# Performance work log

Measured on AMD Instinct MI355X. Metric: run time of the kernel, lower is better.

The kernel has to match this reference:

```python
import jax, jax.numpy as jnp
import numpy as np

# FPMA (Mitchell-style) approximate bf16 multiply: a*b is approximated by
# integer-adding the exponent+mantissa bit fields of the two bf16 operands
# and subtracting the exponent bias offset (0x3F80 for bf16). Sign is XOR of
# sign bits. Underflow is flushed to zero; overflow clamped to max finite.
SIGN_MASK = 0x8000
MAG_MASK = 0x7FFF
BIAS_OFF = 0x3F80  # 127 << 7 (bf16 exponent bias in bit position)
MAX_FINITE = 0x7F7F
CHUNK = 4  # rows of the input processed per scan step (bounds the [C,N,K] intermediate)


def _fpma_matmul(x, w):
    """x: [M,K] bf16, w: [N,K] bf16 -> [M,N] fp32 accumulated approximate products."""
    xb = jax.lax.bitcast_convert_type(x, jnp.uint16).astype(jnp.int32)  # [M,K]
    wb = jax.lax.bitcast_convert_type(w, jnp.uint16).astype(jnp.int32)  # [N,K]
    M, K = xb.shape
    xs, xm = xb & SIGN_MASK, xb & MAG_MASK
    ws, wm = wb & SIGN_MASK, wb & MAG_MASK

    def block(args):
        bs, bm = args  # each [CHUNK, K]
        sign = bs[:, None, :] ^ ws[None]                      # [C,N,K]
        mag = bm[:, None, :] + wm[None] - BIAS_OFF            # approx exp+mant add
        mag = jnp.clip(mag, 0, MAX_FINITE)                    # flush underflow, clamp overflow
        is_zero = (bm[:, None, :] == 0) | (wm[None] == 0)     # exact-zero operands
        bits = jnp.where(is_zero, 0, sign | mag).astype(jnp.uint16)
        prod = jax.lax.bitcast_convert_type(bits, jnp.bfloat16)
        return prod.astype(jnp.float32).sum(-1)               # [C,N] fp32 accumulate

    xs_c = xs.reshape(M // CHUNK, CHUNK, K)
    xm_c = xm.reshape(M // CHUNK, CHUNK, K)
    out = jax.lax.map(block, (xs_c, xm_c))                    # [M//C, C, N]
    return out.reshape(M, -1)


def setup_inputs() -> dict:
    key = jax.random.key(0)
    k1, k2, k3 = jax.random.split(key, 3)
    M, K, N = 4096, 2048, 2048
    input = jax.random.normal(k1, (M, K), dtype=jnp.bfloat16)
    weight = (jax.random.normal(k2, (N, K), dtype=jnp.float32) * 0.02).astype(jnp.bfloat16)
    bias = (jax.random.normal(k3, (1, N), dtype=jnp.float32) * 0.02).astype(jnp.bfloat16)
    return {"input": input, "weight": weight, "bias": bias}


def reference(input, weight, bias):
    orig_shape = input.shape[:-1]
    x = input.reshape(-1, input.shape[-1])
    acc = _fpma_matmul(x, weight)                 # [M,N] fp32
    out = acc.astype(jnp.bfloat16) + bias         # bias added in bf16, as in the kernel wrapper
    return out.reshape(*orig_shape, weight.shape[0])
```

## Files before the change

### kernel.cpp

```cpp
#include <hip/hip_runtime.h>
#include <stdint.h>

typedef unsigned short v2u   __attribute__((ext_vector_type(2)));
typedef unsigned short u16x8 __attribute__((ext_vector_type(8)));
typedef short          s16x8 __attribute__((ext_vector_type(8)));
typedef float          f32x4 __attribute__((ext_vector_type(4)));

#define TM 64
#define TN 64
#define BK 32

__device__ __forceinline__ uint32_t rnd_bf16(float f) {
    uint32_t u = __builtin_bit_cast(uint32_t, f);
    return (u + 0x7FFFu + ((u >> 16) & 1u)) >> 16;
}
__device__ __forceinline__ float bf16_to_f32(uint32_t bits16) {
    return __builtin_bit_cast(float, bits16 << 16);
}

__device__ __forceinline__ uint32_t pack_x(uint32_t w0, uint32_t w1) {
    uint32_t u = (w0 >> 16) | (w1 & 0xFFFF0000u);
    const v2u vfloor = {0x2000, 0x2000};
    v2u m = __builtin_bit_cast(v2u, u & 0x7FFF7FFFu);
    m = __builtin_elementwise_max(m, vfloor);
    uint32_t c = (u & 0x80008000u) ^ 0xC080C080u;
    v2u xp = m + __builtin_bit_cast(v2u, c);
    return __builtin_bit_cast(uint32_t, xp);
}
__device__ __forceinline__ uint32_t pack_w(uint32_t w0, uint32_t w1) {
    uint32_t v = (w0 >> 16) | (w1 & 0xFFFF0000u);
    const v2u vfloor = {0x2000, 0x2000};
    v2u m = __builtin_bit_cast(v2u, v & 0x7FFF7FFFu);
    m = __builtin_elementwise_max(m, vfloor);
    return __builtin_bit_cast(uint32_t, m) | (v & 0x80008000u);
}

__global__ __launch_bounds__(256, 3)
void fpma_gemm(const uint32_t* __restrict__ X,
               const uint32_t* __restrict__ Wt,
               const float*    __restrict__ Bias,
               float* __restrict__ Out,
               int M, int N, int K)
{
    __shared__ uint32_t Xp[2][64 * 16];
    __shared__ uint32_t Wp[2][64 * 16];

    const int tid  = threadIdx.x;
    const int lane = tid & 63;
    const int warp = tid >> 6;
    const int wm = warp >> 1, wn = warp & 1;
    const int m0 = blockIdx.y * TM;
    const int n0 = blockIdx.x * TN;

    const int cc = lane & 15;
    const int q  = lane >> 4;
    const int mi = cc >> 2;
    const int ni = cc & 3;

    const int xrd = (32 * wm + mi) * 16 + ((q ^ mi) << 2);
    int wrd[4];
    #pragma unroll
    for (int t = 0; t < 4; ++t)
        wrd[t] = (32 * wn + ni) * 16 + ((q ^ ni) << 2) + (((q + t) & 3) << 6);

    u16x8 bt[4];
    #pragma unroll
    for (int t = 0; t < 4; ++t) {
        unsigned short v = ((cc >> 2) == ((q + t) & 3)) ? (unsigned short)0x3F80
                                                        : (unsigned short)0;
        bt[t] = (u16x8){v, v, v, v, v, v, v, v};
    }

    const int srow = tid >> 2;
    const int soct = tid & 3;
    const uint32_t* xptr = X  + (size_t)(m0 + srow) * K + soct * 8;
    const uint32_t* wptr = Wt + (size_t)(n0 + srow) * K + soct * 8;
    const int st = srow * 16 + ((soct ^ (srow & 3)) << 2);

    f32x4 acc[8][2];
    #pragma unroll
    for (int a = 0; a < 8; ++a)
        #pragma unroll
        for (int bg = 0; bg < 2; ++bg) acc[a][bg] = (f32x4){0.f, 0.f, 0.f, 0.f};

    {
        uint4 a0 = *(const uint4*)(xptr), a1 = *(const uint4*)(xptr + 4);
        uint4 b0 = *(const uint4*)(wptr), b1 = *(const uint4*)(wptr + 4);
        uint4 px = {pack_x(a0.x, a0.y), pack_x(a0.z, a0.w),
                    pack_x(a1.x, a1.y), pack_x(a1.z, a1.w)};
        uint4 pw = {pack_w(b0.x, b0.y), pack_w(b0.z, b0.w),
                    pack_w(b1.x, b1.y), pack_w(b1.z, b1.w)};
        *(uint4*)&Xp[0][st] = px;
        *(uint4*)&Wp[0][st] = pw;
    }
    uint4 gx0 = {0,0,0,0}, gx1 = {0,0,0,0}, gw0 = {0,0,0,0}, gw1 = {0,0,0,0};
    const int ksteps = K / BK;
    if (ksteps > 1) {
        xptr += BK; wptr += BK;
        gx0 = *(const uint4*)(xptr); gx1 = *(const uint4*)(xptr + 4);
        gw0 = *(const uint4*)(wptr); gw1 = *(const uint4*)(wptr + 4);
    }
    __syncthreads();

    #pragma unroll 1
    for (int kt = 0; kt < ksteps; ++kt) {
        const int cur = kt & 1;
        if (kt + 1 < ksteps) {
            uint4 px = {pack_x(gx0.x, gx0.y), pack_x(gx0.z, gx0.w),
                        pack_x(gx1.x, gx1.y), pack_x(gx1.z, gx1.w)};
            uint4 pw = {pack_w(gw0.x, gw0.y), pack_w(gw0.z, gw0.w),
                        pack_w(gw1.x, gw1.y), pack_w(gw1.z, gw1.w)};
            *(uint4*)&Xp[cur ^ 1][st] = px;
            *(uint4*)&Wp[cur ^ 1][st] = pw;
            if (kt + 2 < ksteps) {
                xptr += BK; wptr += BK;
                gx0 = *(const uint4*)(xptr); gx1 = *(const uint4*)(xptr + 4);
                gw0 = *(const uint4*)(wptr); gw1 = *(const uint4*)(wptr + 4);
            }
        }

        u16x8 xf[8];
        #pragma unroll
        for (int a = 0; a < 8; ++a)
            xf[a] = __builtin_bit_cast(u16x8,
                        *(const uint4*)&Xp[cur][xrd + a * 64]);

        __builtin_amdgcn_s_setprio(1);
        #pragma unroll
        for (int bg = 0; bg < 2; ++bg) {
            u16x8 wf[4];
            #pragma unroll
            for (int t = 0; t < 4; ++t)
                wf[t] = __builtin_bit_cast(u16x8,
                            *(const uint4*)&Wp[cur][wrd[t] + bg * 256]);
            #pragma unroll
            for (int t = 0; t < 4; ++t)
                #pragma unroll
                for (int a = 0; a < 8; ++a) {
                    u16x8 p = xf[a] + wf[t];
                    acc[a][bg] = __builtin_amdgcn_mfma_f32_16x16x32_bf16(
                        __builtin_bit_cast(s16x8, p),
                        __builtin_bit_cast(s16x8, bt[t]),
                        acc[a][bg], 0, 0, 0);
                }
        }
        __builtin_amdgcn_s_setprio(0);
        __syncthreads();
    }

    const int g = cc >> 2;
    f32x4 bias_[2];
    #pragma unroll
    for (int bg = 0; bg < 2; ++bg)
        bias_[bg] = *(const f32x4*)&Bias[n0 + 32 * wn + 16 * bg + 4 * g];

    #pragma unroll
    for (int a = 0; a < 8; ++a) {
        if ((cc & 3) == (a & 3)) {
            #pragma unroll
            for (int bg = 0; bg < 2; ++bg) {
                float o[4];
                #pragma unroll
                for (int j = 0; j < 4; ++j)
                    o[j] = bf16_to_f32(rnd_bf16(
                               bf16_to_f32(rnd_bf16(acc[a][bg][j])) + bias_[bg][j]));
                const size_t row = (size_t)(m0 + 32 * wm + 4 * a + q) * N;
                *(float4*)&Out[row + n0 + 32 * wn + 16 * bg + 4 * g] =
                    make_float4(o[0], o[1], o[2], o[3]);
            }
        }
    }
}

extern "C" void kernel_launch(void* const* d_in, const int* in_sizes, int n_in,
                              void* d_out, int out_size, void* d_ws, size_t ws_size,
                              hipStream_t stream) {
    (void)n_in; (void)d_ws; (void)ws_size; (void)out_size;
    const uint32_t* X = (const uint32_t*)d_in[0];
    const uint32_t* W = (const uint32_t*)d_in[1];
    const float*    B = (const float*)d_in[2];
    float* O = (float*)d_out;

    int N = in_sizes[2];
    int K = (N > 0) ? in_sizes[1] / N : 0;
    int M = (K > 0) ? in_sizes[0] / K : 0;
    if (N <= 0 || K <= 0 || M <= 0 ||
        (long long)N * K != (long long)in_sizes[1] ||
        (long long)M * K != (long long)in_sizes[0] ||
        (M % TM) || (N % TN) || (K % BK)) {
        M = 4096; K = 2048; N = 2048;
    }

    dim3 grid(N / TN, M / TM);
    fpma_gemm<<<grid, 256, 0, stream>>>(X, W, B, O, M, N, K);
}
```

Before: 570.7 us.

## Prepack operands in workspace and stream them into LDS with global_load_lds

```diff
diff --git a/kernel.cpp b/kernel.cpp
--- a/kernel.cpp
+++ b/kernel.cpp
@@ -35,6 +35,21 @@
     return __builtin_bit_cast(uint32_t, m) | (v & 0x80008000u);
 }
 
+__global__ void pack_kernel(const uint32_t* __restrict__ in,
+                            uint32_t* __restrict__ out, int n4, int mode)
+{
+    int i = blockIdx.x * blockDim.x + threadIdx.x;
+    const int stride = gridDim.x * blockDim.x;
+    for (; i < n4; i += stride) {
+        uint4 v = ((const uint4*)in)[i];
+        uint2 o;
+        if (mode == 0) { o.x = pack_x(v.x, v.y); o.y = pack_x(v.z, v.w); }
+        else           { o.x = pack_w(v.x, v.y); o.y = pack_w(v.z, v.w); }
+        ((uint2*)out)[i] = o;
+    }
+}
+
+template<bool PRE>
 __global__ __launch_bounds__(256, 3)
 void fpma_gemm(const uint32_t* __restrict__ X,
                const uint32_t* __restrict__ Wt,
@@ -73,32 +88,38 @@
 
     const int srow = tid >> 2;
     const int soct = tid & 3;
+    const int ksteps = K / BK;
+
+    f32x4 acc[8][2];
+    #pragma unroll
+    for (int a = 0; a < 8; ++a)
+        #pragma unroll
+        for (int bg = 0; bg < 2; ++bg) acc[a][bg] = (f32x4){0.f, 0.f, 0.f, 0.f};
+
+    const int Kp = K >> 1;
+    const uint32_t* xsrc = X  + (size_t)(m0 + srow) * Kp + ((soct ^ (srow & 3)) << 2);
+    const uint32_t* wsrc = Wt + (size_t)(n0 + srow) * Kp + ((soct ^ (srow & 3)) << 2);
     const uint32_t* xptr = X  + (size_t)(m0 + srow) * K + soct * 8;
     const uint32_t* wptr = Wt + (size_t)(n0 + srow) * K + soct * 8;
     const int st = srow * 16 + ((soct ^ (srow & 3)) << 2);
-
-    f32x4 acc[8][2];
-    #pragma unroll
-    for (int a = 0; a < 8; ++a)
-        #pragma unroll
-        for (int bg = 0; bg < 2; ++bg) acc[a][bg] = (f32x4){0.f, 0.f, 0.f, 0.f};
-
-    {
+    uint4 gx0 = {0,0,0,0}, gx1 = {0,0,0,0}, gw0 = {0,0,0,0}, gw1 = {0,0,0,0};
+
+    if constexpr (PRE) {
+        __builtin_amdgcn_global_load_lds(xsrc, &Xp[0][tid << 2], 16, 0, 0);
+        __builtin_amdgcn_global_load_lds(wsrc, &Wp[0][tid << 2], 16, 0, 0);
+        xsrc += 16; wsrc += 16;
+    } else {
         uint4 a0 = *(const uint4*)(xptr), a1 = *(const uint4*)(xptr + 4);
         uint4 b0 = *(const uint4*)(wptr), b1 = *(const uint4*)(wptr + 4);
-        uint4 px = {pack_x(a0.x, a0.y), pack_x(a0.z, a0.w),
-                    pack_x(a1.x, a1.y), pack_x(a1.z, a1.w)};
-        uint4 pw = {pack_w(b0.x, b0.y), pack_w(b0.z, b0.w),
-                    pack_w(b1.x, b1.y), pack_w(b1.z, b1.w)};
-        *(uint4*)&Xp[0][st] = px;
-        *(uint4*)&Wp[0][st] = pw;
-    }
-    uint4 gx0 = {0,0,0,0}, gx1 = {0,0,0,0}, gw0 = {0,0,0,0}, gw1 = {0,0,0,0};
-    const int ksteps = K / BK;
-    if (ksteps > 1) {
-        xptr += BK; wptr += BK;
-        gx0 = *(const uint4*)(xptr); gx1 = *(const uint4*)(xptr + 4);
-        gw0 = *(const uint4*)(wptr); gw1 = *(const uint4*)(wptr + 4);
+        *(uint4*)&Xp[0][st] = (uint4){pack_x(a0.x,a0.y), pack_x(a0.z,a0.w),
+                                      pack_x(a1.x,a1.y), pack_x(a1.z,a1.w)};
+        *(uint4*)&Wp[0][st] = (uint4){pack_w(b0.x,b0.y), pack_w(b0.z,b0.w),
+                                      pack_w(b1.x,b1.y), pack_w(b1.z,b1.w)};
+        if (ksteps > 1) {
+            xptr += BK; wptr += BK;
+            gx0 = *(const uint4*)(xptr); gx1 = *(const uint4*)(xptr + 4);
+            gw0 = *(const uint4*)(wptr); gw1 = *(const uint4*)(wptr + 4);
+        }
     }
     __syncthreads();
 
@@ -106,16 +127,20 @@
     for (int kt = 0; kt < ksteps; ++kt) {
         const int cur = kt & 1;
         if (kt + 1 < ksteps) {
-            uint4 px = {pack_x(gx0.x, gx0.y), pack_x(gx0.z, gx0.w),
-                        pack_x(gx1.x, gx1.y), pack_x(gx1.z, gx1.w)};
-            uint4 pw = {pack_w(gw0.x, gw0.y), pack_w(gw0.z, gw0.w),
-                        pack_w(gw1.x, gw1.y), pack_w(gw1.z, gw1.w)};
-            *(uint4*)&Xp[cur ^ 1][st] = px;
-            *(uint4*)&Wp[cur ^ 1][st] = pw;
-            if (kt + 2 < ksteps) {
-                xptr += BK; wptr += BK;
-                gx0 = *(const uint4*)(xptr); gx1 = *(const uint4*)(xptr + 4);
-                gw0 = *(const uint4*)(wptr); gw1 = *(const uint4*)(wptr + 4);
+            if constexpr (PRE) {
+                __builtin_amdgcn_global_load_lds(xsrc, &Xp[cur ^ 1][tid << 2], 16, 0, 0);
+                __builtin_amdgcn_global_load_lds(wsrc, &Wp[cur ^ 1][tid << 2], 16, 0, 0);
+                xsrc += 16; wsrc += 16;
+            } else {
+                *(uint4*)&Xp[cur ^ 1][st] = (uint4){pack_x(gx0.x,gx0.y), pack_x(gx0.z,gx0.w),
+                                                    pack_x(gx1.x,gx1.y), pack_x(gx1.z,gx1.w)};
+                *(uint4*)&Wp[cur ^ 1][st] = (uint4){pack_w(gw0.x,gw0.y), pack_w(gw0.z,gw0.w),
+                                                    pack_w(gw1.x,gw1.y), pack_w(gw1.z,gw1.w)};
+                if (kt + 2 < ksteps) {
+                    xptr += BK; wptr += BK;
+                    gx0 = *(const uint4*)(xptr); gx1 = *(const uint4*)(xptr + 4);
+                    gw0 = *(const uint4*)(wptr); gw1 = *(const uint4*)(wptr + 4);
+                }
             }
         }
 
@@ -175,7 +200,7 @@
 extern "C" void kernel_launch(void* const* d_in, const int* in_sizes, int n_in,
                               void* d_out, int out_size, void* d_ws, size_t ws_size,
                               hipStream_t stream) {
-    (void)n_in; (void)d_ws; (void)ws_size; (void)out_size;
+    (void)n_in; (void)out_size;
     const uint32_t* X = (const uint32_t*)d_in[0];
     const uint32_t* W = (const uint32_t*)d_in[1];
     const float*    B = (const float*)d_in[2];
@@ -187,10 +212,22 @@
     if (N <= 0 || K <= 0 || M <= 0 ||
         (long long)N * K != (long long)in_sizes[1] ||
         (long long)M * K != (long long)in_sizes[0] ||
-        (M % TM) || (N % TN) || (K % BK)) {
+        (M % TM) || (N % TN) || (K % BK) || (K % 8)) {
         M = 4096; K = 2048; N = 2048;
     }
 
+    const size_t xq_words = (size_t)M * (K / 2);
+    const size_t wq_words = (size_t)N * (K / 2);
+    const size_t need = (xq_words + wq_words) * 4;
+
     dim3 grid(N / TN, M / TM);
-    fpma_gemm<<<grid, 256, 0, stream>>>(X, W, B, O, M, N, K);
-}
+    if (d_ws != nullptr && ws_size >= need) {
+        uint32_t* Xq = (uint32_t*)d_ws;
+        uint32_t* Wq = Xq + xq_words;
+        pack_kernel<<<1024, 256, 0, stream>>>(X, Xq, (int)(xq_words / 2), 0);
+        pack_kernel<<<1024, 256, 0, stream>>>(W, Wq, (int)(wq_words / 2), 1);
+        fpma_gemm<true><<<grid, 256, 0, stream>>>(Xq, Wq, B, O, M, N, K);
+    } else {
+        fpma_gemm<false><<<grid, 256, 0, stream>>>(X, W, B, O, M, N, K);
+    }
+}
```

Measured after the change: 526.9 us. -7.7%, faster.
